# Kernel optimization log

Measured on AMD Instinct MI355X. Metric: run time of the kernel, lower is better.

## Reference

```python
import jax, jax.numpy as jnp
import numpy as np

N = 200_000          # nodes
E = 6_400_000        # directed edges (before self loops)
F_IN, F_OUT = 20, 10
NEG_SLOPE = 0.2      # PyG GATConv default
BN_EPS = 1e-5


def setup_inputs() -> dict:
    key = jax.random.key(0)
    ks = jax.random.split(key, 20)
    s = 0.1
    return {
        "h": jax.random.normal(ks[0], (N, F_IN), jnp.float32),
        "edge_index": jax.random.randint(ks[1], (2, E), 0, N, dtype=jnp.int64),
        "edge_weight": jax.random.uniform(ks[2], (E, 1), dtype=jnp.float32),
        # BatchNorm1d(20) affine params
        "bn_w": jnp.ones((F_IN,), jnp.float32),
        "bn_b": jnp.zeros((F_IN,), jnp.float32),
        # GATConv params (heads=1): lin (no bias), att vectors, edge lin, output bias
        "W": jax.random.normal(ks[3], (F_OUT, F_IN), jnp.float32) * s,
        "att_src": jax.random.normal(ks[4], (F_OUT,), jnp.float32) * s,
        "att_dst": jax.random.normal(ks[5], (F_OUT,), jnp.float32) * s,
        "att_edge": jax.random.normal(ks[6], (F_OUT,), jnp.float32) * s,
        "W_edge": jax.random.normal(ks[7], (F_OUT, 1), jnp.float32) * s,
        "bias": jax.random.normal(ks[8], (F_OUT,), jnp.float32) * s,
        # dense MLP
        "fc1_w": jax.random.normal(ks[9], (F_OUT, F_OUT), jnp.float32) * s,
        "fc1_b": jnp.zeros((F_OUT,), jnp.float32),
        "fc2_w": jax.random.normal(ks[10], (F_OUT, F_OUT), jnp.float32) * s,
        "fc2_b": jnp.zeros((F_OUT,), jnp.float32),
        "fc3_w": jax.random.normal(ks[11], (F_OUT, F_OUT), jnp.float32) * s,
        "fc3_b": jnp.zeros((F_OUT,), jnp.float32),
    }


def reference(h, edge_index, edge_weight, bn_w, bn_b, W, att_src, att_dst,
              att_edge, W_edge, bias, fc1_w, fc1_b, fc2_w, fc2_b, fc3_w, fc3_b):
    # --- BatchNorm1d (training mode: batch stats, biased variance) ---
    mu = h.mean(axis=0)
    var = jnp.var(h, axis=0)
    xn = (h - mu) * jax.lax.rsqrt(var + BN_EPS) * bn_w + bn_b   # [N, 20]

    # --- GATConv (heads=1, edge_dim=1, add_self_loops, fill_value='mean') ---
    xp = xn @ W.T                       # [N, 10] projected node features
    a_s = xp @ att_src                  # [N] per-node source attention term
    a_d = xp @ att_dst                  # [N] per-node dest attention term

    loop = jnp.arange(N, dtype=edge_index.dtype)
    src = jnp.concatenate([edge_index[0], loop])          # [E+N]
    dst = jnp.concatenate([edge_index[1], loop])          # [E+N]
    loop_attr = jnp.broadcast_to(edge_weight.mean(axis=0), (N, 1))
    ea = jnp.concatenate([edge_weight, loop_attr], axis=0)  # [E+N, 1]

    a_e = (ea @ W_edge.T) @ att_edge                       # [E+N]
    logits = jax.nn.leaky_relu(a_s[src] + a_d[dst] + a_e, NEG_SLOPE)

    # segment softmax over destination neighborhoods (every node has a self loop)
    m = jax.ops.segment_max(logits, dst, num_segments=N)
    ex = jnp.exp(logits - m[dst])
    denom = jax.ops.segment_sum(ex, dst, num_segments=N)
    alpha = ex / denom[dst]                                # [E+N]

    msg = xp[src] * alpha[:, None]                         # [E+N, 10]
    out = jax.ops.segment_sum(msg, dst, num_segments=N) + bias  # [N, 10]

    embeddings = jax.nn.relu(out)
    y = jax.nn.relu(out @ fc1_w.T + fc1_b)
    y = jax.nn.relu(y @ fc2_w.T + fc2_b)
    y = y @ fc3_w.T + fc3_b
    return embeddings, y
```

## Files before the change

kernel.cpp:

```cpp
#include <hip/hip_runtime.h>
#include <hip/hip_fp16.h>

#define NN 200000
#define NE 6400000
#define F_IN 20
#define F_OUT 10
#define NEG_SLOPE 0.2f
#define BN_EPS 1e-5f

#define NPB 256
#define NBUCK 782
#define CHUNK 8192
#define NBLK 782
#define SB 512
#define SSB 1024
#define SNPT (CHUNK / SSB)
#define SZ (NBUCK * NBLK)
#define SCANB 1024
#define G1 ((SZ + SCANB - 1) / SCANB)
#define PREB 120
#define RT 1024
#define MAXB 9216
#define CNPT ((MAXB + RT - 1) / RT)

#define OFF_C      41
#define OFF_LOOPAE 42
#define OFF_SCALE  64
#define OFF_SHIFT  84
#define OFF_PART   128
#define OFF_PEW    (OFF_PART + PREB * 40)
#define OFF_AD     (OFF_PEW + PREB)
#define OFF_XPA    (OFF_AD + NN)
#define OFF_XPB    (OFF_XPA + 4 * NN)
#define OFF_SCN    (OFF_XPB + 2 * NN)
#define OFF_BS     (OFF_SCN + SZ + 1)
#define OFF_M      (((OFF_BS + 1024) + 1) & ~1)
#define OFF_REC    OFF_M

typedef unsigned long long u64;

__global__ void __launch_bounds__(SB) k_pre(
        const float* __restrict__ h, const float* __restrict__ ew,
        const int* __restrict__ ei, float* __restrict__ part,
        float* __restrict__ pew, int* __restrict__ M) {
    int t = threadIdx.x;
    if (blockIdx.x < PREB) {
        float s[F_IN], q[F_IN];
#pragma unroll
        for (int f = 0; f < F_IN; ++f) { s[f] = 0.f; q[f] = 0.f; }
        for (int i = blockIdx.x * SB + t; i < NN; i += PREB * SB) {
            const float4* row = (const float4*)(h + (size_t)i * F_IN);
#pragma unroll
            for (int v = 0; v < 5; ++v) {
                float4 x = row[v];
                int f = v * 4;
                s[f+0] += x.x; q[f+0] += x.x * x.x;
                s[f+1] += x.y; q[f+1] += x.y * x.y;
                s[f+2] += x.z; q[f+2] += x.z * x.z;
                s[f+3] += x.w; q[f+3] += x.w * x.w;
            }
        }
#pragma unroll
        for (int f = 0; f < F_IN; ++f)
            for (int o = 32; o > 0; o >>= 1) {
                s[f] += __shfl_down(s[f], o);
                q[f] += __shfl_down(q[f], o);
            }
        __shared__ float red[8][40];
        int wave = t >> 6, lane = t & 63;
        if (lane == 0) {
#pragma unroll
            for (int f = 0; f < F_IN; ++f) { red[wave][f] = s[f]; red[wave][F_IN + f] = q[f]; }
        }
        __syncthreads();
        if (t < 40) {
            float a = 0.f;
#pragma unroll
            for (int w8 = 0; w8 < 8; ++w8) a += red[w8][t];
            part[blockIdx.x * 40 + t] = a;
        }
    } else if (blockIdx.x < 2 * PREB) {
        int g = blockIdx.x - PREB;
        float s = 0.f;
        const float4* e4 = (const float4*)ew;
        const int n4 = NE / 4;
        for (int i = g * SB + t; i < n4; i += PREB * SB) {
            float4 x = e4[i];
            s += x.x + x.y + x.z + x.w;
        }
        for (int o = 32; o > 0; o >>= 1) s += __shfl_down(s, o);
        __shared__ float red2[8];
        if ((t & 63) == 0) red2[t >> 6] = s;
        __syncthreads();
        if (t == 0) {
            float a = 0.f;
#pragma unroll
            for (int w8 = 0; w8 < 8; ++w8) a += red2[w8];
            pew[g] = a;
        }
    } else {
        __shared__ int hist[NBUCK];
        int blk = blockIdx.x - 2 * PREB;
        for (int i = t; i < NBUCK; i += SB) hist[i] = 0;
        __syncthreads();
        int base = blk * CHUNK;
        int lim = NE - base; if (lim > CHUNK) lim = CHUNK;
        for (int j = t; j < lim; j += SB) {
            int dst = ei[NE + base + j];
            atomicAdd(&hist[dst >> 8], 1);
        }
        __syncthreads();
        for (int i = t; i < NBUCK; i += SB) M[i * NBLK + blk] = hist[i];
    }
}

__global__ void k_params(const float* __restrict__ bn_w, const float* __restrict__ bn_b,
                         const float* __restrict__ W_edge, const float* __restrict__ att_edge,
                         const float* __restrict__ part, const float* __restrict__ pew,
                         float* __restrict__ ws) {
    __shared__ float col[40];
    __shared__ float ews;
    int t = threadIdx.x;
    if (t < 40) {
        float s = 0.f;
#pragma unroll 8
        for (int b = 0; b < PREB; ++b) s += part[b * 40 + t];
        col[t] = s;
    }
    if (t == 40) {
        float s = 0.f;
#pragma unroll 8
        for (int b = 0; b < PREB; ++b) s += pew[b];
        ews = s;
    }
    __syncthreads();
    if (t < F_IN) {
        float mu  = col[t] / (float)NN;
        float var = col[F_IN + t] / (float)NN - mu * mu;
        float sc  = bn_w[t] * rsqrtf(var + BN_EPS);
        ws[OFF_SCALE + t] = sc;
        ws[OFF_SHIFT + t] = bn_b[t] - mu * sc;
    }
    if (t == 63) {
        float c = 0.f;
#pragma unroll
        for (int k = 0; k < F_OUT; ++k) c += W_edge[k] * att_edge[k];
        ws[OFF_C] = c;
        ws[OFF_LOOPAE] = c * (ews / (float)NE);
    }
}

__global__ void k_node(const float* __restrict__ h, const float* __restrict__ W,
                       const float* __restrict__ att_src, const float* __restrict__ att_dst,
                       const float* __restrict__ ws_ro, __half* __restrict__ xpa,
                       float* __restrict__ xpb, float* __restrict__ a_d) {
    __shared__ float sW[F_OUT * F_IN], sAs[F_OUT], sAd[F_OUT], sSc[F_IN], sSh[F_IN];
    int t = threadIdx.x;
    if (t < F_OUT * F_IN) sW[t] = W[t];
    if (t < F_OUT) { sAs[t] = att_src[t]; sAd[t] = att_dst[t]; }
    if (t >= 224 && t < 224 + F_IN) {
        sSc[t - 224] = ws_ro[OFF_SCALE + (t - 224)];
        sSh[t - 224] = ws_ro[OFF_SHIFT + (t - 224)];
    }
    __syncthreads();
    int i = blockIdx.x * blockDim.x + t;
    if (i >= NN) return;
    float xn[F_IN];
    const float4* row = (const float4*)(h + (size_t)i * F_IN);
#pragma unroll
    for (int v = 0; v < 5; ++v) {
        float4 x = row[v];
        int f = v * 4;
        xn[f+0] = x.x * sSc[f+0] + sSh[f+0];
        xn[f+1] = x.y * sSc[f+1] + sSh[f+1];
        xn[f+2] = x.z * sSc[f+2] + sSh[f+2];
        xn[f+3] = x.w * sSc[f+3] + sSh[f+3];
    }
    float acc[F_OUT];
    float as = 0.f, ad = 0.f;
#pragma unroll
    for (int k = 0; k < F_OUT; ++k) {
        float a = 0.f;
#pragma unroll
        for (int f = 0; f < F_IN; ++f) a += sW[k * F_IN + f] * xn[f];
        acc[k] = a;
        as += a * sAs[k];
        ad += a * sAd[k];
    }
    __half2 h01 = __floats2half2_rn(acc[0], acc[1]);
    __half2 h23 = __floats2half2_rn(acc[2], acc[3]);
    __half2 h45 = __floats2half2_rn(acc[4], acc[5]);
    __half2 h67 = __floats2half2_rn(acc[6], acc[7]);
    __half2 h89 = __floats2half2_rn(acc[8], acc[9]);
    uint4 U;
    U.x = *(unsigned*)&h01; U.y = *(unsigned*)&h23;
    U.z = *(unsigned*)&h45; U.w = *(unsigned*)&h67;
    *(uint4*)(xpa + (size_t)i * 8) = U;
    uint2 V;
    V.x = *(unsigned*)&h89;
    V.y = __float_as_uint(as);
    *(uint2*)(xpb + (size_t)i * 2) = V;
    a_d[i] = ad;
}

__global__ void k_scan1(const int* __restrict__ M, int* __restrict__ SCN,
                        int* __restrict__ BS) {
    __shared__ int tmp[SCANB];
    int t = threadIdx.x, g = blockIdx.x;
    int idx = g * SCANB + t;
    int v = (idx < SZ) ? M[idx] : 0;
    tmp[t] = v;
    __syncthreads();
    for (int off = 1; off < SCANB; off <<= 1) {
        int x = (t >= off) ? tmp[t - off] : 0;
        __syncthreads();
        tmp[t] += x;
        __syncthreads();
    }
    if (idx < SZ) SCN[idx] = tmp[t] - v;
    if (t == SCANB - 1) BS[g] = tmp[t];
}

__global__ void k_scan2(int* __restrict__ BS) {
    __shared__ int tmp[SCANB];
    int t = threadIdx.x;
    int v = (t < G1) ? BS[t] : 0;
    tmp[t] = v;
    __syncthreads();
    for (int off = 1; off < SCANB; off <<= 1) {
        int x = (t >= off) ? tmp[t - off] : 0;
        __syncthreads();
        tmp[t] += x;
        __syncthreads();
    }
    if (t < G1) BS[t] = tmp[t] - v;
}

__global__ void __launch_bounds__(SSB) k_scatter(
        const int* __restrict__ ei, const float* __restrict__ ew,
        const int* __restrict__ SCN, const int* __restrict__ BS,
        u64* __restrict__ rec) {
    __shared__ u64 sBuf[CHUNK];
    __shared__ int sScan[1024];
    __shared__ int sCur[NBUCK];
    __shared__ int sBase[NBUCK];
    int t = threadIdx.x, blk = blockIdx.x;
    sScan[t] = 0;
    for (int i = t; i < NBUCK; i += SSB) {
        int idx = i * NBLK + blk;
        sBase[i] = SCN[idx] + BS[idx >> 10];
    }
    __syncthreads();
    int base = blk * CHUNK;
    int lim = NE - base; if (lim > CHUNK) lim = CHUNK;
    u64 r[SNPT]; int bk[SNPT];
#pragma unroll
    for (int k = 0; k < SNPT; ++k) {
        int j = t + k * SSB;
        bk[k] = -1;
        if (j < lim) {
            int e = base + j;
            int src = __builtin_nontemporal_load(ei + e);
            int dst = ei[NE + e];
            float w  = __builtin_nontemporal_load(ew + e);
            int b = dst >> 8;
            bk[k] = b;
            r[k] = ((u64)__float_as_uint(w) << 32) |
                   (u64)(((unsigned)src << 8) | (unsigned)(dst & (NPB - 1)));
            atomicAdd(&sScan[b], 1);
        }
    }
    __syncthreads();
    for (int d = 1; d < 1024; d <<= 1) {
        int idx = (t + 1) * (d << 1) - 1;
        if (idx < 1024) sScan[idx] += sScan[idx - d];
        __syncthreads();
    }
    if (t == 0) sScan[1023] = 0;
    __syncthreads();
    for (int d = 512; d >= 1; d >>= 1) {
        int idx = (t + 1) * (d << 1) - 1;
        if (idx < 1024) {
            int x = sScan[idx - d];
            sScan[idx - d] = sScan[idx];
            sScan[idx] += x;
        }
        __syncthreads();
    }
    for (int i = t; i < NBUCK; i += SSB) sCur[i] = sScan[i];
    __syncthreads();
#pragma unroll
    for (int k = 0; k < SNPT; ++k) {
        if (bk[k] >= 0) {
            int p = atomicAdd(&sCur[bk[k]], 1);
            sBuf[p] = r[k];
        }
    }
    __syncthreads();
    int grp = t >> 3, lane = t & 7;
    for (int b = grp; b < NBUCK; b += SSB / 8) {
        int st = sScan[b];
        int len = sScan[b + 1] - st;
        int gb = sBase[b];
        for (int k2 = lane; k2 < len; k2 += 8)
            rec[gb + k2] = sBuf[st + k2];
    }
}

__global__ void __launch_bounds__(RT, 8) k_creduce(
        const float* __restrict__ ws_ro, const int* __restrict__ SCN,
        const int* __restrict__ BS,
        const u64* __restrict__ rec, const __half* __restrict__ xpa,
        const float* __restrict__ xpb, const float* __restrict__ a_d,
        const float* __restrict__ bias,
        const float* __restrict__ fc1w, const float* __restrict__ fc1b,
        const float* __restrict__ fc2w, const float* __restrict__ fc2b,
        const float* __restrict__ fc3w, const float* __restrict__ fc3b,
        float* __restrict__ out) {
    __shared__ u64 sBuf[MAXB];
    __shared__ int sHist[NPB];
    __shared__ int sOff[NPB + 1];
    __shared__ float s1[100], s2[100], s3[100], sb[F_OUT], sb1[F_OUT], sb2[F_OUT], sb3[F_OUT];
    int t = threadIdx.x, b = blockIdx.x;
    if (t < NPB) sHist[t] = 0;
    if (t < 100) { s1[t] = fc1w[t]; s2[t] = fc2w[t]; s3[t] = fc3w[t]; }
    if (t >= 256 && t < 256 + F_OUT) {
        int k = t - 256;
        sb[k] = bias[k]; sb1[k] = fc1b[k]; sb2[k] = fc2b[k]; sb3[k] = fc3b[k];
    }
    __syncthreads();
    int i0 = b * NBLK;
    int start = SCN[i0] + BS[i0 >> 10];
    int end;
    if (b == NBUCK - 1) end = NE;
    else { int i1 = (b + 1) * NBLK; end = SCN[i1] + BS[i1 >> 10]; }
    int cnt = end - start;
    if (cnt > MAXB) cnt = MAXB;
    u64 r[CNPT];
#pragma unroll
    for (int k = 0; k < CNPT; ++k) {
        int i = t + k * RT;
        if (i < cnt) {
            r[k] = __builtin_nontemporal_load(rec + start + i);
            atomicAdd(&sHist[(unsigned)r[k] & (NPB - 1u)], 1);
        }
    }
    __syncthreads();
    int v = (t < NPB) ? sHist[t] : 0;
    for (int off = 1; off < NPB; off <<= 1) {
        int x = (t >= off && t < NPB) ? sHist[t - off] : 0;
        __syncthreads();
        if (t < NPB) sHist[t] += x;
        __syncthreads();
    }
    if (t < NPB) { sOff[t + 1] = sHist[t]; sHist[t] -= v; }
    if (t == 0) sOff[0] = 0;
    __syncthreads();
#pragma unroll
    for (int k = 0; k < CNPT; ++k) {
        int i = t + k * RT;
        if (i < cnt) {
            int p = atomicAdd(&sHist[(unsigned)r[k] & (NPB - 1u)], 1);
            if (p < MAXB) sBuf[p] = r[k];
        }
    }
    __syncthreads();
    int node = t & (NPB - 1);
    int quarter = t >> 8;
    int gnode = b * NPB + node;
    float adn = (gnode < NN) ? a_d[gnode] : 0.f;
    float c = ws_ro[OFF_C];
    const uint4* xpa4 = (const uint4*)xpa;
    const uint2* xpb2 = (const uint2*)xpb;
    int myStart = sOff[node];
    int e0 = sOff[node + 1];
    float den = 0.f;
    float num[F_OUT];
#pragma unroll
    for (int k = 0; k < F_OUT; ++k) num[k] = 0.f;
    int j = myStart + quarter;
    for (; j + 12 < e0; j += 16) {
        u64 r1 = sBuf[j];
        u64 r2 = sBuf[j + 4];
        u64 r3 = sBuf[j + 8];
        u64 r4 = sBuf[j + 12];
        unsigned i1 = (unsigned)r1 >> 8, i2 = (unsigned)r2 >> 8;
        unsigned i3 = (unsigned)r3 >> 8, i4 = (unsigned)r4 >> 8;
        uint4 A1 = xpa4[i1]; uint4 A2 = xpa4[i2];
        uint4 A3 = xpa4[i3]; uint4 A4 = xpa4[i4];
        uint2 B1 = xpb2[i1]; uint2 B2 = xpb2[i2];
        uint2 B3 = xpb2[i3]; uint2 B4 = xpb2[i4];
        float l1 = __uint_as_float(B1.y) + adn + c * __uint_as_float((unsigned)(r1 >> 32));
        float l2 = __uint_as_float(B2.y) + adn + c * __uint_as_float((unsigned)(r2 >> 32));
        float l3 = __uint_as_float(B3.y) + adn + c * __uint_as_float((unsigned)(r3 >> 32));
        float l4 = __uint_as_float(B4.y) + adn + c * __uint_as_float((unsigned)(r4 >> 32));
        l1 = l1 > 0.f ? l1 : NEG_SLOPE * l1;
        l2 = l2 > 0.f ? l2 : NEG_SLOPE * l2;
        l3 = l3 > 0.f ? l3 : NEG_SLOPE * l3;
        l4 = l4 > 0.f ? l4 : NEG_SLOPE * l4;
        float e1 = __expf(l1), e2 = __expf(l2), e3 = __expf(l3), e4 = __expf(l4);
        float2 f0 = __half22float2(*(const __half2*)&A1.x);
        float2 f1 = __half22float2(*(const __half2*)&A1.y);
        float2 f2 = __half22float2(*(const __half2*)&A1.z);
        float2 f3 = __half22float2(*(const __half2*)&A1.w);
        float2 f4 = __half22float2(*(const __half2*)&B1.x);
        float2 g0 = __half22float2(*(const __half2*)&A2.x);
        float2 g1 = __half22float2(*(const __half2*)&A2.y);
        float2 g2 = __half22float2(*(const __half2*)&A2.z);
        float2 g3 = __half22float2(*(const __half2*)&A2.w);
        float2 g4 = __half22float2(*(const __half2*)&B2.x);
        float2 h0 = __half22float2(*(const __half2*)&A3.x);
        float2 h1 = __half22float2(*(const __half2*)&A3.y);
        float2 h2 = __half22float2(*(const __half2*)&A3.z);
        float2 h3 = __half22float2(*(const __half2*)&A3.w);
        float2 h4 = __half22float2(*(const __half2*)&B3.x);
        float2 k0 = __half22float2(*(const __half2*)&A4.x);
        float2 k1 = __half22float2(*(const __half2*)&A4.y);
        float2 k2 = __half22float2(*(const __half2*)&A4.z);
        float2 k3 = __half22float2(*(const __half2*)&A4.w);
        float2 k4 = __half22float2(*(const __half2*)&B4.x);
        den += (e1 + e2) + (e3 + e4);
        num[0] += e1 * f0.x + e2 * g0.x + e3 * h0.x + e4 * k0.x;
        num[1] += e1 * f0.y + e2 * g0.y + e3 * h0.y + e4 * k0.y;
        num[2] += e1 * f1.x + e2 * g1.x + e3 * h1.x + e4 * k1.x;
        num[3] += e1 * f1.y + e2 * g1.y + e3 * h1.y + e4 * k1.y;
        num[4] += e1 * f2.x + e2 * g2.x + e3 * h2.x + e4 * k2.x;
        num[5] += e1 * f2.y + e2 * g2.y + e3 * h2.y + e4 * k2.y;
        num[6] += e1 * f3.x + e2 * g3.x + e3 * h3.x + e4 * k3.x;
        num[7] += e1 * f3.y + e2 * g3.y + e3 * h3.y + e4 * k3.y;
        num[8] += e1 * f4.x + e2 * g4.x + e3 * h4.x + e4 * k4.x;
        num[9] += e1 * f4.y + e2 * g4.y + e3 * h4.y + e4 * k4.y;
    }
    for (; j < e0; j += 4) {
        u64 r1 = sBuf[j];
        unsigned i1 = (unsigned)r1 >> 8;
        uint4 A = xpa4[i1];
        uint2 B = xpb2[i1];
        float l1 = __uint_as_float(B.y) + adn + c * __uint_as_float((unsigned)(r1 >> 32));
        l1 = l1 > 0.f ? l1 : NEG_SLOPE * l1;
        float e1 = __expf(l1);
        float2 f0 = __half22float2(*(const __half2*)&A.x);
        float2 f1 = __half22float2(*(const __half2*)&A.y);
        float2 f2 = __half22float2(*(const __half2*)&A.z);
        float2 f3 = __half22float2(*(const __half2*)&A.w);
        float2 f4 = __half22float2(*(const __half2*)&B.x);
        den += e1;
        num[0] += e1 * f0.x; num[1] += e1 * f0.y;
        num[2] += e1 * f1.x; num[3] += e1 * f1.y;
        num[4] += e1 * f2.x; num[5] += e1 * f2.y;
        num[6] += e1 * f3.x; num[7] += e1 * f3.y;
        num[8] += e1 * f4.x; num[9] += e1 * f4.y;
    }
    __syncthreads();
    float* sP = (float*)sBuf;
    if (quarter) {
        float* p = sP + (node * 3 + (quarter - 1)) * 11;
        p[0] = den;
#pragma unroll
        for (int k = 0; k < F_OUT; ++k) p[1 + k] = num[k];
    }
    __syncthreads();
    if (quarter) return;
#pragma unroll
    for (int q = 0; q < 3; ++q) {
        const float* p = sP + (node * 3 + q) * 11;
        den += p[0];
#pragma unroll
        for (int k = 0; k < F_OUT; ++k) num[k] += p[1 + k];
    }

    if (gnode >= NN) return;
    uint4 An = xpa4[gnode];
    uint2 Bn = xpb2[gnode];
    float l = __uint_as_float(Bn.y) + adn + ws_ro[OFF_LOOPAE];
    l = l > 0.f ? l : NEG_SLOPE * l;
    float exs = __expf(l);
    float inv = 1.0f / (den + exs);
    float xn[F_OUT];
    {
        float2 f0 = __half22float2(*(const __half2*)&An.x);
        float2 f1 = __half22float2(*(const __half2*)&An.y);
        float2 f2 = __half22float2(*(const __half2*)&An.z);
        float2 f3 = __half22float2(*(const __half2*)&An.w);
        float2 f4 = __half22float2(*(const __half2*)&Bn.x);
        xn[0]=f0.x; xn[1]=f0.y; xn[2]=f1.x; xn[3]=f1.y; xn[4]=f2.x;
        xn[5]=f2.y; xn[6]=f3.x; xn[7]=f3.y; xn[8]=f4.x; xn[9]=f4.y;
    }
    float o[F_OUT], y1[F_OUT], y2[F_OUT];
#pragma unroll
    for (int k = 0; k < F_OUT; ++k) {
        o[k] = (num[k] + exs * xn[k]) * inv + sb[k];
        out[(size_t)gnode * F_OUT + k] = fmaxf(o[k], 0.f);
    }
#pragma unroll
    for (int k = 0; k < F_OUT; ++k) {
        float a = sb1[k];
#pragma unroll
        for (int jj = 0; jj < F_OUT; ++jj) a += s1[k * F_OUT + jj] * o[jj];
        y1[k] = fmaxf(a, 0.f);
    }
#pragma unroll
    for (int k = 0; k < F_OUT; ++k) {
        float a = sb2[k];
#pragma unroll
        for (int jj = 0; jj < F_OUT; ++jj) a += s2[k * F_OUT + jj] * y1[jj];
        y2[k] = fmaxf(a, 0.f);
    }
#pragma unroll
    for (int k = 0; k < F_OUT; ++k) {
        float a = sb3[k];
#pragma unroll
        for (int jj = 0; jj < F_OUT; ++jj) a += s3[k * F_OUT + jj] * y2[jj];
        out[(size_t)NN * F_OUT + (size_t)gnode * F_OUT + k] = a;
    }
}

extern "C" void kernel_launch(void* const* d_in, const int* in_sizes, int n_in,
                              void* d_out, int out_size, void* d_ws, size_t ws_size,
                              hipStream_t stream) {
    const float* h        = (const float*)d_in[0];
    const int*   ei       = (const int*)  d_in[1];
    const float* ew       = (const float*)d_in[2];
    const float* bn_w     = (const float*)d_in[3];
    const float* bn_b     = (const float*)d_in[4];
    const float* W        = (const float*)d_in[5];
    const float* att_src  = (const float*)d_in[6];
    const float* att_dst  = (const float*)d_in[7];
    const float* att_edge = (const float*)d_in[8];
    const float* W_edge   = (const float*)d_in[9];
    const float* bias     = (const float*)d_in[10];
    const float* fc1w     = (const float*)d_in[11];
    const float* fc1b     = (const float*)d_in[12];
    const float* fc2w     = (const float*)d_in[13];
    const float* fc2b     = (const float*)d_in[14];
    const float* fc3w     = (const float*)d_in[15];
    const float* fc3b     = (const float*)d_in[16];
    float* ws  = (float*)d_ws;
    int*   wsi = (int*)d_ws;
    float* out = (float*)d_out;
    __half* xpa = (__half*)(ws + OFF_XPA);
    float*  xpb = ws + OFF_XPB;

    k_pre   <<<2 * PREB + NBLK, SB, 0, stream>>>(h, ew, ei, ws + OFF_PART,
                                                 ws + OFF_PEW, wsi + OFF_M);
    k_params<<<1, 64, 0, stream>>>(bn_w, bn_b, W_edge, att_edge,
                                   ws + OFF_PART, ws + OFF_PEW, ws);
    k_node  <<<(NN + 255) / 256, 256, 0, stream>>>(h, W, att_src, att_dst, ws,
                                                   xpa, xpb, ws + OFF_AD);
    k_scan1 <<<G1, SCANB, 0, stream>>>(wsi + OFF_M, wsi + OFF_SCN, wsi + OFF_BS);
    k_scan2 <<<1, SCANB, 0, stream>>>(wsi + OFF_BS);
    k_scatter<<<NBLK, SSB, 0, stream>>>(ei, ew, wsi + OFF_SCN, wsi + OFF_BS,
                                        (u64*)(wsi + OFF_REC));
    k_creduce<<<NBUCK, RT, 0, stream>>>(ws, wsi + OFF_SCN, wsi + OFF_BS,
                                        (const u64*)(wsi + OFF_REC),
                                        xpa, xpb, ws + OFF_AD,
                                        bias, fc1w, fc1b, fc2w, fc2b, fc3w, fc3b, out);
}
```

Measured before the change: 329.5 us.

## Fold edge-weight sum into scatter and BN param finalize into node kernel

The separate edge-weight reduction pass in k_pre is removed. Per-block edge-weight partial sums are now taken in k_scatter, which already loads every weight. The single-block k_params kernel is eliminated: each k_node block redundantly reduces the BN partials and edge-weight partials itself, and block 0 writes the loop attention constant. This saves a full 25.6 MB read of edge weights and one kernel launch, but adds redundant per-block reduction work in k_node and reorders kernels so k_node runs after the scatter.

```diff
diff --git a/kernel.cpp b/kernel.cpp
--- a/kernel.cpp
+++ b/kernel.cpp
@@ -25,12 +25,10 @@
 
 #define OFF_C      41
 #define OFF_LOOPAE 42
-#define OFF_SCALE  64
-#define OFF_SHIFT  84
 #define OFF_PART   128
 #define OFF_PEW    (OFF_PART + PREB * 40)
-#define OFF_AD     (OFF_PEW + PREB)
-#define OFF_XPA    (OFF_AD + NN)
+#define OFF_AD     (OFF_PEW + NBLK)
+#define OFF_XPA    (((OFF_AD + NN) + 3) & ~3)
 #define OFF_XPB    (OFF_XPA + 4 * NN)
 #define OFF_SCN    (OFF_XPB + 2 * NN)
 #define OFF_BS     (OFF_SCN + SZ + 1)
@@ -40,9 +38,8 @@
 typedef unsigned long long u64;
 
 __global__ void __launch_bounds__(SB) k_pre(
-        const float* __restrict__ h, const float* __restrict__ ew,
-        const int* __restrict__ ei, float* __restrict__ part,
-        float* __restrict__ pew, int* __restrict__ M) {
+        const float* __restrict__ h, const int* __restrict__ ei,
+        float* __restrict__ part, int* __restrict__ M) {
     int t = threadIdx.x;
     if (blockIdx.x < PREB) {
         float s[F_IN], q[F_IN];
@@ -79,28 +76,9 @@
             for (int w8 = 0; w8 < 8; ++w8) a += red[w8][t];
             part[blockIdx.x * 40 + t] = a;
         }
-    } else if (blockIdx.x < 2 * PREB) {
-        int g = blockIdx.x - PREB;
-        float s = 0.f;
-        const float4* e4 = (const float4*)ew;
-        const int n4 = NE / 4;
-        for (int i = g * SB + t; i < n4; i += PREB * SB) {
-            float4 x = e4[i];
-            s += x.x + x.y + x.z + x.w;
-        }
-        for (int o = 32; o > 0; o >>= 1) s += __shfl_down(s, o);
-        __shared__ float red2[8];
-        if ((t & 63) == 0) red2[t >> 6] = s;
-        __syncthreads();
-        if (t == 0) {
-            float a = 0.f;
-#pragma unroll
-            for (int w8 = 0; w8 < 8; ++w8) a += red2[w8];
-            pew[g] = a;
-        }
     } else {
         __shared__ int hist[NBUCK];
-        int blk = blockIdx.x - 2 * PREB;
+        int blk = blockIdx.x - PREB;
         for (int i = t; i < NBUCK; i += SB) hist[i] = 0;
         __syncthreads();
         int base = blk * CHUNK;
@@ -114,53 +92,160 @@
     }
 }
 
-__global__ void k_params(const float* __restrict__ bn_w, const float* __restrict__ bn_b,
-                         const float* __restrict__ W_edge, const float* __restrict__ att_edge,
-                         const float* __restrict__ part, const float* __restrict__ pew,
-                         float* __restrict__ ws) {
+__global__ void k_scan1(const int* __restrict__ M, int* __restrict__ SCN,
+                        int* __restrict__ BS) {
+    __shared__ int tmp[SCANB];
+    int t = threadIdx.x, g = blockIdx.x;
+    int idx = g * SCANB + t;
+    int v = (idx < SZ) ? M[idx] : 0;
+    tmp[t] = v;
+    __syncthreads();
+    for (int off = 1; off < SCANB; off <<= 1) {
+        int x = (t >= off) ? tmp[t - off] : 0;
+        __syncthreads();
+        tmp[t] += x;
+        __syncthreads();
+    }
+    if (idx < SZ) SCN[idx] = tmp[t] - v;
+    if (t == SCANB - 1) BS[g] = tmp[t];
+}
+
+__global__ void k_scan2(int* __restrict__ BS) {
+    __shared__ int tmp[SCANB];
+    int t = threadIdx.x;
+    int v = (t < G1) ? BS[t] : 0;
+    tmp[t] = v;
+    __syncthreads();
+    for (int off = 1; off < SCANB; off <<= 1) {
+        int x = (t >= off) ? tmp[t - off] : 0;
+        __syncthreads();
+        tmp[t] += x;
+        __syncthreads();
+    }
+    if (t < G1) BS[t] = tmp[t] - v;
+}
+
+__global__ void __launch_bounds__(SSB) k_scatter(
+        const int* __restrict__ ei, const float* __restrict__ ew,
+        const int* __restrict__ SCN, const int* __restrict__ BS,
+        u64* __restrict__ rec, float* __restrict__ pew) {
+    __shared__ u64 sBuf[CHUNK];
+    __shared__ int sScan[1024];
+    __shared__ int sCur[NBUCK];
+    __shared__ int sBase[NBUCK];
+    __shared__ float redw[16];
+    int t = threadIdx.x, blk = blockIdx.x;
+    sScan[t] = 0;
+    for (int i = t; i < NBUCK; i += SSB) {
+        int idx = i * NBLK + blk;
+        sBase[i] = SCN[idx] + BS[idx >> 10];
+    }
+    __syncthreads();
+    int base = blk * CHUNK;
+    int lim = NE - base; if (lim > CHUNK) lim = CHUNK;
+    u64 r[SNPT]; int bk[SNPT];
+    float es = 0.f;
+#pragma unroll
+    for (int k = 0; k < SNPT; ++k) {
+        int j = t + k * SSB;
+        bk[k] = -1;
+        if (j < lim) {
+            int e = base + j;
+            int src = __builtin_nontemporal_load(ei + e);
+            int dst = ei[NE + e];
+            float w  = __builtin_nontemporal_load(ew + e);
+            es += w;
+            int b = dst >> 8;
+            bk[k] = b;
+            r[k] = ((u64)__float_as_uint(w) << 32) |
+                   (u64)(((unsigned)src << 8) | (unsigned)(dst & (NPB - 1)));
+            atomicAdd(&sScan[b], 1);
+        }
+    }
+    for (int o = 32; o > 0; o >>= 1) es += __shfl_down(es, o);
+    if ((t & 63) == 0) redw[t >> 6] = es;
+    __syncthreads();
+    if (t == 0) {
+        float a = 0.f;
+#pragma unroll
+        for (int w16 = 0; w16 < 16; ++w16) a += redw[w16];
+        pew[blk] = a;
+    }
+    for (int d = 1; d < 1024; d <<= 1) {
+        int idx = (t + 1) * (d << 1) - 1;
+        if (idx < 1024) sScan[idx] += sScan[idx - d];
+        __syncthreads();
+    }
+    if (t == 0) sScan[1023] = 0;
+    __syncthreads();
+    for (int d = 512; d >= 1; d >>= 1) {
+        int idx = (t + 1) * (d << 1) - 1;
+        if (idx < 1024) {
+            int x = sScan[idx - d];
+            sScan[idx - d] = sScan[idx];
+            sScan[idx] += x;
+        }
+        __syncthreads();
+    }
+    for (int i = t; i < NBUCK; i += SSB) sCur[i] = sScan[i];
+    __syncthreads();
+#pragma unroll
+    for (int k = 0; k < SNPT; ++k) {
+        if (bk[k] >= 0) {
+            int p = atomicAdd(&sCur[bk[k]], 1);
+            sBuf[p] = r[k];
+        }
+    }
+    __syncthreads();
+    int grp = t >> 3, lane = t & 7;
+    for (int b = grp; b < NBUCK; b += SSB / 8) {
+        int st = sScan[b];
+        int len = sScan[b + 1] - st;
+        int gb = sBase[b];
+        for (int k2 = lane; k2 < len; k2 += 8)
+            rec[gb + k2] = sBuf[st + k2];
+    }
+}
+
+__global__ void k_node(const float* __restrict__ h, const float* __restrict__ W,
+                       const float* __restrict__ att_src, const float* __restrict__ att_dst,
+                       const float* __restrict__ bn_w, const float* __restrict__ bn_b,
+                       const float* __restrict__ W_edge, const float* __restrict__ att_edge,
+                       const float* __restrict__ part, const float* __restrict__ pew,
+                       float* __restrict__ ws, __half* __restrict__ xpa,
+                       float* __restrict__ xpb, float* __restrict__ a_d) {
+    __shared__ float sW[F_OUT * F_IN], sAs[F_OUT], sAd[F_OUT], sSc[F_IN], sSh[F_IN];
     __shared__ float col[40];
-    __shared__ float ews;
+    __shared__ float redw[4];
     int t = threadIdx.x;
-    if (t < 40) {
+    if (t < F_OUT * F_IN) sW[t] = W[t];
+    if (t < F_OUT) { sAs[t] = att_src[t]; sAd[t] = att_dst[t]; }
+    if (t >= 200 && t < 240) {
+        int f = t - 200;
         float s = 0.f;
 #pragma unroll 8
-        for (int b = 0; b < PREB; ++b) s += part[b * 40 + t];
-        col[t] = s;
-    }
-    if (t == 40) {
-        float s = 0.f;
-#pragma unroll 8
-        for (int b = 0; b < PREB; ++b) s += pew[b];
-        ews = s;
-    }
+        for (int b = 0; b < PREB; ++b) s += part[b * 40 + f];
+        col[f] = s;
+    }
+    float es = 0.f;
+    for (int i = t; i < NBLK; i += 256) es += pew[i];
+    for (int o = 32; o > 0; o >>= 1) es += __shfl_down(es, o);
+    if ((t & 63) == 0) redw[t >> 6] = es;
     __syncthreads();
     if (t < F_IN) {
         float mu  = col[t] / (float)NN;
         float var = col[F_IN + t] / (float)NN - mu * mu;
         float sc  = bn_w[t] * rsqrtf(var + BN_EPS);
-        ws[OFF_SCALE + t] = sc;
-        ws[OFF_SHIFT + t] = bn_b[t] - mu * sc;
-    }
-    if (t == 63) {
+        sSc[t] = sc;
+        sSh[t] = bn_b[t] - mu * sc;
+    }
+    if (t == 63 && blockIdx.x == 0) {
+        float ews = redw[0] + redw[1] + redw[2] + redw[3];
         float c = 0.f;
 #pragma unroll
         for (int k = 0; k < F_OUT; ++k) c += W_edge[k] * att_edge[k];
         ws[OFF_C] = c;
         ws[OFF_LOOPAE] = c * (ews / (float)NE);
-    }
-}
-
-__global__ void k_node(const float* __restrict__ h, const float* __restrict__ W,
-                       const float* __restrict__ att_src, const float* __restrict__ att_dst,
-                       const float* __restrict__ ws_ro, __half* __restrict__ xpa,
-                       float* __restrict__ xpb, float* __restrict__ a_d) {
-    __shared__ float sW[F_OUT * F_IN], sAs[F_OUT], sAd[F_OUT], sSc[F_IN], sSh[F_IN];
-    int t = threadIdx.x;
-    if (t < F_OUT * F_IN) sW[t] = W[t];
-    if (t < F_OUT) { sAs[t] = att_src[t]; sAd[t] = att_dst[t]; }
-    if (t >= 224 && t < 224 + F_IN) {
-        sSc[t - 224] = ws_ro[OFF_SCALE + (t - 224)];
-        sSh[t - 224] = ws_ro[OFF_SHIFT + (t - 224)];
     }
     __syncthreads();
     int i = blockIdx.x * blockDim.x + t;
@@ -201,110 +286,6 @@
     V.y = __float_as_uint(as);
     *(uint2*)(xpb + (size_t)i * 2) = V;
     a_d[i] = ad;
-}
-
-__global__ void k_scan1(const int* __restrict__ M, int* __restrict__ SCN,
-                        int* __restrict__ BS) {
-    __shared__ int tmp[SCANB];
-    int t = threadIdx.x, g = blockIdx.x;
-    int idx = g * SCANB + t;
-    int v = (idx < SZ) ? M[idx] : 0;
-    tmp[t] = v;
-    __syncthreads();
-    for (int off = 1; off < SCANB; off <<= 1) {
-        int x = (t >= off) ? tmp[t - off] : 0;
-        __syncthreads();
-        tmp[t] += x;
-        __syncthreads();
-    }
-    if (idx < SZ) SCN[idx] = tmp[t] - v;
-    if (t == SCANB - 1) BS[g] = tmp[t];
-}
-
-__global__ void k_scan2(int* __restrict__ BS) {
-    __shared__ int tmp[SCANB];
-    int t = threadIdx.x;
-    int v = (t < G1) ? BS[t] : 0;
-    tmp[t] = v;
-    __syncthreads();
-    for (int off = 1; off < SCANB; off <<= 1) {
-        int x = (t >= off) ? tmp[t - off] : 0;
-        __syncthreads();
-        tmp[t] += x;
-        __syncthreads();
-    }
-    if (t < G1) BS[t] = tmp[t] - v;
-}
-
-__global__ void __launch_bounds__(SSB) k_scatter(
-        const int* __restrict__ ei, const float* __restrict__ ew,
-        const int* __restrict__ SCN, const int* __restrict__ BS,
-        u64* __restrict__ rec) {
-    __shared__ u64 sBuf[CHUNK];
-    __shared__ int sScan[1024];
-    __shared__ int sCur[NBUCK];
-    __shared__ int sBase[NBUCK];
-    int t = threadIdx.x, blk = blockIdx.x;
-    sScan[t] = 0;
-    for (int i = t; i < NBUCK; i += SSB) {
-        int idx = i * NBLK + blk;
-        sBase[i] = SCN[idx] + BS[idx >> 10];
-    }
-    __syncthreads();
-    int base = blk * CHUNK;
-    int lim = NE - base; if (lim > CHUNK) lim = CHUNK;
-    u64 r[SNPT]; int bk[SNPT];
-#pragma unroll
-    for (int k = 0; k < SNPT; ++k) {
-        int j = t + k * SSB;
-        bk[k] = -1;
-        if (j < lim) {
-            int e = base + j;
-            int src = __builtin_nontemporal_load(ei + e);
-            int dst = ei[NE + e];
-            float w  = __builtin_nontemporal_load(ew + e);
-            int b = dst >> 8;
-            bk[k] = b;
-            r[k] = ((u64)__float_as_uint(w) << 32) |
-                   (u64)(((unsigned)src << 8) | (unsigned)(dst & (NPB - 1)));
-            atomicAdd(&sScan[b], 1);
-        }
-    }
-    __syncthreads();
-    for (int d = 1; d < 1024; d <<= 1) {
-        int idx = (t + 1) * (d << 1) - 1;
-        if (idx < 1024) sScan[idx] += sScan[idx - d];
-        __syncthreads();
-    }
-    if (t == 0) sScan[1023] = 0;
-    __syncthreads();
-    for (int d = 512; d >= 1; d >>= 1) {
-        int idx = (t + 1) * (d << 1) - 1;
-        if (idx < 1024) {
-            int x = sScan[idx - d];
-            sScan[idx - d] = sScan[idx];
-            sScan[idx] += x;
-        }
-        __syncthreads();
-    }
-    for (int i = t; i < NBUCK; i += SSB) sCur[i] = sScan[i];
-    __syncthreads();
-#pragma unroll
-    for (int k = 0; k < SNPT; ++k) {
-        if (bk[k] >= 0) {
-            int p = atomicAdd(&sCur[bk[k]], 1);
-            sBuf[p] = r[k];
-        }
-    }
-    __syncthreads();
-    int grp = t >> 3, lane = t & 7;
-    for (int b = grp; b < NBUCK; b += SSB / 8) {
-        int st = sScan[b];
-        int len = sScan[b + 1] - st;
-        int gb = sBase[b];
-        for (int k2 = lane; k2 < len; k2 += 8)
-            rec[gb + k2] = sBuf[st + k2];
-    }
 }
 
 __global__ void __launch_bounds__(RT, 8) k_creduce(
@@ -541,16 +522,15 @@
     __half* xpa = (__half*)(ws + OFF_XPA);
     float*  xpb = ws + OFF_XPB;
 
-    k_pre   <<<2 * PREB + NBLK, SB, 0, stream>>>(h, ew, ei, ws + OFF_PART,
-                                                 ws + OFF_PEW, wsi + OFF_M);
-    k_params<<<1, 64, 0, stream>>>(bn_w, bn_b, W_edge, att_edge,
-                                   ws + OFF_PART, ws + OFF_PEW, ws);
-    k_node  <<<(NN + 255) / 256, 256, 0, stream>>>(h, W, att_src, att_dst, ws,
-                                                   xpa, xpb, ws + OFF_AD);
+    k_pre   <<<PREB + NBLK, SB, 0, stream>>>(h, ei, ws + OFF_PART, wsi + OFF_M);
     k_scan1 <<<G1, SCANB, 0, stream>>>(wsi + OFF_M, wsi + OFF_SCN, wsi + OFF_BS);
     k_scan2 <<<1, SCANB, 0, stream>>>(wsi + OFF_BS);
     k_scatter<<<NBLK, SSB, 0, stream>>>(ei, ew, wsi + OFF_SCN, wsi + OFF_BS,
-                                        (u64*)(wsi + OFF_REC));
+                                        (u64*)(wsi + OFF_REC), ws + OFF_PEW);
+    k_node  <<<(NN + 255) / 256, 256, 0, stream>>>(h, W, att_src, att_dst,
+                                                   bn_w, bn_b, W_edge, att_edge,
+                                                   ws + OFF_PART, ws + OFF_PEW,
+                                                   ws, xpa, xpb, ws + OFF_AD);
     k_creduce<<<NBUCK, RT, 0, stream>>>(ws, wsi + OFF_SCN, wsi + OFF_BS,
                                         (const u64*)(wsi + OFF_REC),
                                         xpa, xpb, ws + OFF_AD,
```

Result: faster. 319.1 us (-3.1%).
